# Optimization experiments

Measured on AMD Instinct MI355X. Metric: run time of the kernel, lower is better.

The kernel has to match this reference:

```python
import math
import jax, jax.numpy as jnp
import numpy as np

N_FREQS = 16
MAX_PERIOD = 4096.0
INJECTION_SCALE = 1.0


def setup_inputs() -> dict:
    key = jax.random.key(0)
    ks = jax.random.split(key, 5)
    B, L, D, K = 4, 8192, 1024, 2
    read_in = K * 2 * N_FREQS  # 64
    x = jax.random.normal(ks[0], (B, L, D), dtype=jnp.float32)
    # Linear weights stored as (in, out) so y = x @ W + b (== torch x @ W.T + b)
    inc_w = jax.random.normal(ks[1], (D, K), dtype=jnp.float32) * 0.02
    inc_b = jnp.full((K,), -2.0, dtype=jnp.float32)   # nn.init.constant_(inc_proj.bias, -2.0)
    reset_w = jax.random.normal(ks[2], (D, K), dtype=jnp.float32) * 0.02
    reset_b = jnp.full((K,), -5.0, dtype=jnp.float32)  # nn.init.constant_(reset_proj.bias, -5.0)
    read_w = jax.random.normal(ks[3], (read_in, D), dtype=jnp.float32) * 0.02
    read_b = jnp.zeros((D,), dtype=jnp.float32)
    return {"x": x, "inc_w": inc_w, "inc_b": inc_b, "reset_w": reset_w,
            "reset_b": reset_b, "read_w": read_w, "read_b": read_b}


def reference(x, inc_w, inc_b, reset_w, reset_b, read_w, read_b):
    # Gates from hidden state
    inc_logits = x @ inc_w + inc_b        # (B, L, K)
    reset_logits = x @ reset_w + reset_b  # (B, L, K)
    inc = jax.nn.sigmoid(inc_logits)
    keep = 1.0 - jax.nn.sigmoid(reset_logits)

    # Diagonal linear recurrence c[t] = keep[t]*c[t-1] + inc[t]
    # expressed as an associative scan over affine maps f(x) = k*x + i.
    def combine(left, right):
        kl, il = left
        kr, ir = right
        return (kl * kr, ir + kr * il)

    _, counters = jax.lax.associative_scan(combine, (keep, inc), axis=1)  # (B, L, K)

    # Sinusoidal readout: (B, L, K) -> (B, L, K*2*n_freqs)
    freqs = jnp.exp(jnp.linspace(0.0, math.log(MAX_PERIOD), N_FREQS)).astype(x.dtype)
    sc = counters[..., None] / freqs                       # (B, L, K, F)
    emb = jnp.concatenate([jnp.sin(sc), jnp.cos(sc)], -1)  # (B, L, K, 2F)
    B, L, K, _ = emb.shape
    emb = emb.reshape(B, L, K * 2 * N_FREQS)

    injection = INJECTION_SCALE * (emb @ read_w + read_b)  # (B, L, d_model)
    return injection, inc_logits, counters
```

## Files before the change

kernel.cpp:

```cpp
#include <hip/hip_runtime.h>

#define B_    4
#define L_    8192
#define D_    1024
#define ROWS_ 32768
#define NCH_  128

typedef __attribute__((ext_vector_type(8))) short  short8;
typedef __attribute__((ext_vector_type(4))) float  floatx4;

__device__ __forceinline__ unsigned short f2bf(float f){
  unsigned int u = __float_as_uint(f);
  u += 0x7fffu + ((u >> 16) & 1u);
  return (unsigned short)(u >> 16);
}

__global__ __launch_bounds__(512) void k_gates(
    const float* __restrict__ x,
    const float* __restrict__ inc_w, const float* __restrict__ inc_b,
    const float* __restrict__ reset_w, const float* __restrict__ reset_b,
    float* __restrict__ out_incl,
    float* __restrict__ cl, float* __restrict__ kc,
    float* __restrict__ sumP, float* __restrict__ sumQ,
    const float* __restrict__ read_w, unsigned short* __restrict__ Bt)
{
  const int blk  = blockIdx.x;
  if (blk >= 512){
    const int idx0 = ((blk - 512)*512 + threadIdx.x)*4;
    const int n  = idx0 >> 6;
    const int kk = idx0 & 63;
    ushort4 v;
    v.x = f2bf(read_w[(size_t)(kk+0)*D_ + n]);
    v.y = f2bf(read_w[(size_t)(kk+1)*D_ + n]);
    v.z = f2bf(read_w[(size_t)(kk+2)*D_ + n]);
    v.w = f2bf(read_w[(size_t)(kk+3)*D_ + n]);
    *(ushort4*)(Bt + idx0) = v;
    return;
  }

  __shared__ float s_keep[128];
  __shared__ float s_inc[128];
  const int b    = blk >> 7;
  const int ch   = blk & 127;
  const int tid  = threadIdx.x;
  const int w    = tid >> 6;
  const int lane = tid & 63;

  float4 wia[4], wib[4], wra[4], wrb[4];
  #pragma unroll
  for (int i = 0; i < 4; ++i){
    const int d0 = i*256 + lane*4;
    const float4* pi = (const float4*)(inc_w + d0*2);
    wia[i] = pi[0]; wib[i] = pi[1];
    const float4* pr = (const float4*)(reset_w + d0*2);
    wra[i] = pr[0]; wrb[i] = pr[1];
  }
  const float bi0 = inc_b[0], bi1 = inc_b[1];
  const float br0 = reset_b[0], br1 = reset_b[1];

  const int row0 = b*L_ + ch*64 + w*8;
  floatx4 xc[4], xn[4];
  {
    const floatx4* xr = (const floatx4*)(x + (size_t)row0 * D_);
    #pragma unroll
    for (int i = 0; i < 4; ++i) xc[i] = __builtin_nontemporal_load(xr + i*64 + lane);
  }
  #pragma unroll
  for (int r = 0; r < 8; ++r){
    if (r < 7){
      const floatx4* xr = (const floatx4*)(x + (size_t)(row0 + r + 1) * D_);
      #pragma unroll
      for (int i = 0; i < 4; ++i) xn[i] = __builtin_nontemporal_load(xr + i*64 + lane);
    }
    float ai0=0.f, ai1=0.f, ar0=0.f, ar1=0.f;
    #pragma unroll
    for (int i = 0; i < 4; ++i){
      const floatx4 v = xc[i];
      ai0 += v[0]*wia[i].x + v[1]*wia[i].z + v[2]*wib[i].x + v[3]*wib[i].z;
      ai1 += v[0]*wia[i].y + v[1]*wia[i].w + v[2]*wib[i].y + v[3]*wib[i].w;
      ar0 += v[0]*wra[i].x + v[1]*wra[i].z + v[2]*wrb[i].x + v[3]*wrb[i].z;
      ar1 += v[0]*wra[i].y + v[1]*wra[i].w + v[2]*wrb[i].y + v[3]*wrb[i].w;
    }
    #pragma unroll
    for (int m = 1; m < 64; m <<= 1){
      ai0 += __shfl_xor(ai0, m);
      ai1 += __shfl_xor(ai1, m);
      ar0 += __shfl_xor(ar0, m);
      ar1 += __shfl_xor(ar1, m);
    }
    if (lane == 0){
      const int row = row0 + r;
      const float il0 = ai0 + bi0, il1 = ai1 + bi1;
      const float rl0 = ar0 + br0, rl1 = ar1 + br1;
      out_incl[(size_t)row*2 + 0] = il0;
      out_incl[(size_t)row*2 + 1] = il1;
      const int lr = w*8 + r;
      s_inc [lr*2+0] = 1.f / (1.f + __expf(-il0));
      s_inc [lr*2+1] = 1.f / (1.f + __expf(-il1));
      s_keep[lr*2+0] = 1.f - 1.f / (1.f + __expf(-rl0));
      s_keep[lr*2+1] = 1.f - 1.f / (1.f + __expf(-rl1));
    }
    #pragma unroll
    for (int i = 0; i < 4; ++i) xc[i] = xn[i];
  }
  __syncthreads();

  if (tid < 128){
    const int k = w;
    float P = s_keep[lane*2 + k];
    float Q = s_inc [lane*2 + k];
    #pragma unroll
    for (int ofs = 1; ofs < 64; ofs <<= 1){
      const float Pp = __shfl_up(P, ofs);
      const float Qp = __shfl_up(Q, ofs);
      if (lane >= ofs){ Q = Q + P * Qp; P = P * Pp; }
    }
    const int row = b*L_ + ch*64 + lane;
    cl[(size_t)row*2 + k] = Q;
    kc[(size_t)row*2 + k] = P;
    if (lane == 63){
      const int seq = b*2 + k;
      sumP[seq*NCH_ + ch] = P;
      sumQ[seq*NCH_ + ch] = Q;
    }
  }
}

__global__ __launch_bounds__(256) void k_fused(
    const float* __restrict__ cl, const float* __restrict__ kc,
    const float* __restrict__ sumP, const float* __restrict__ sumQ,
    const unsigned short* __restrict__ Bt,
    const float* __restrict__ read_b,
    float* __restrict__ out_cnt, float* __restrict__ out)
{
  __shared__ float s_carry[2];
  const int tid  = threadIdx.x;
  const int w    = tid >> 6;
  const int lane = tid & 63;
  const int stripe = blockIdx.x >> 1;
  const int half   = blockIdx.x & 1;
  const int rowBase0 = stripe * 64;
  const int b  = rowBase0 >> 13;
  const int ch = stripe & 127;
  const int m    = lane & 15;
  const int quad = lane >> 4;
  const int colBase = half*512 + w*128;

  if (w < 2){
    const int seq = b*2 + w;
    const float* P0 = sumP + seq*NCH_;
    const float* Q0 = sumQ + seq*NCH_;
    float P = P0[lane], Q = Q0[lane];
    #pragma unroll
    for (int ofs = 1; ofs < 64; ofs <<= 1){
      const float Pp = __shfl_up(P, ofs);
      const float Qp = __shfl_up(Q, ofs);
      if (lane >= ofs){ Q = Q + P * Qp; P = P * Pp; }
    }
    float carry = 0.f;
    if (ch > 0 && ch <= 64) carry = __shfl(Q, ch-1);
    const float Qc = __shfl(Q, 63);
    float P2 = P0[64 + lane], Q2 = Q0[64 + lane];
    #pragma unroll
    for (int ofs = 1; ofs < 64; ofs <<= 1){
      const float Pp = __shfl_up(P2, ofs);
      const float Qp = __shfl_up(Q2, ofs);
      if (lane >= ofs){ Q2 = Q2 + P2 * Qp; P2 = P2 * Pp; }
    }
    Q2 = Q2 + P2 * Qc;
    if (ch >= 65) carry = __shfl(Q2, ch-65);
    if (lane == 0) s_carry[w] = carry;
  }
  __syncthreads();
  const float carry0 = s_carry[0];
  const float carry1 = s_carry[1];

  short8 b0[8], b1[8];
  float  bias[8];
  #pragma unroll
  for (int ct = 0; ct < 8; ++ct){
    const int n = colBase + ct*16 + m;
    const short8* bp = (const short8*)(Bt + (size_t)n * 64);
    b0[ct]  = bp[quad];
    b1[ct]  = bp[4 + quad];
    bias[ct] = read_b[n];
  }

  const float TWO_PI_INV = 0.15915494309189535f;
  const float STEP = 0.5743491774985175f;
  const float INVF0 = (quad & 1) ? 0.011841535573494211f  : 1.0f;
  const bool use_cos = (quad >> 1) != 0;

  #pragma unroll
  for (int rt = 0; rt < 4; ++rt){
    const int rowBase = rowBase0 + rt*16;
    const int row = rowBase + m;

    const float2 clv = *(const float2*)(cl + (size_t)row*2);
    const float2 kcv = *(const float2*)(kc + (size_t)row*2);
    const float c0 = clv.x + kcv.x * carry0;
    const float c1 = clv.y + kcv.y * carry1;
    if (half == 0 && w == 0 && lane < 16){
      ((float2*)out_cnt)[row] = make_float2(c0, c1);
    }

    float invf = INVF0;
    short8 a0, a1;
    #pragma unroll
    for (int j = 0; j < 8; ++j){
      float r0 = c0 * invf * TWO_PI_INV; r0 -= floorf(r0);
      float r1 = c1 * invf * TWO_PI_INV; r1 -= floorf(r1);
      const float e0 = use_cos ? __builtin_amdgcn_cosf(r0) : __builtin_amdgcn_sinf(r0);
      const float e1 = use_cos ? __builtin_amdgcn_cosf(r1) : __builtin_amdgcn_sinf(r1);
      a0[j] = (short)f2bf(e0);
      a1[j] = (short)f2bf(e1);
      invf *= STEP;
    }

    floatx4 acc[8];
    #pragma unroll
    for (int ct = 0; ct < 8; ++ct) acc[ct] = (floatx4){0.f,0.f,0.f,0.f};
    #pragma unroll
    for (int ct = 0; ct < 8; ++ct){
      acc[ct] = __builtin_amdgcn_mfma_f32_16x16x32_bf16(a0, b0[ct], acc[ct], 0, 0, 0);
      acc[ct] = __builtin_amdgcn_mfma_f32_16x16x32_bf16(a1, b1[ct], acc[ct], 0, 0, 0);
    }

    #pragma unroll
    for (int ct = 0; ct < 8; ++ct){
      const int col = colBase + ct*16 + m;
      #pragma unroll
      for (int r = 0; r < 4; ++r){
        const int orow = rowBase + quad*4 + r;
        __builtin_nontemporal_store(acc[ct][r] + bias[ct], &out[(size_t)orow*D_ + col]);
      }
    }
  }
}

extern "C" void kernel_launch(void* const* d_in, const int* in_sizes, int n_in,
                              void* d_out, int out_size, void* d_ws, size_t ws_size,
                              hipStream_t stream) {
  const float* x       = (const float*)d_in[0];
  const float* inc_w   = (const float*)d_in[1];
  const float* inc_b   = (const float*)d_in[2];
  const float* reset_w = (const float*)d_in[3];
  const float* reset_b = (const float*)d_in[4];
  const float* read_w  = (const float*)d_in[5];
  const float* read_b  = (const float*)d_in[6];

  float* out      = (float*)d_out;
  float* out_incl = out + (size_t)ROWS_ * D_;
  float* out_cnt  = out_incl + ROWS_ * 2;

  char* ws = (char*)d_ws;
  float* cl    = (float*)(ws + 0);
  float* kc    = (float*)(ws + 262144);
  float* sumP  = (float*)(ws + 524288);
  float* sumQ  = (float*)(ws + 528384);
  unsigned short* Bt  = (unsigned short*)(ws + 532480);

  k_gates<<<dim3(544),  dim3(512), 0, stream>>>(x, inc_w, inc_b, reset_w, reset_b,
                                                out_incl, cl, kc, sumP, sumQ,
                                                read_w, Bt);
  k_fused<<<dim3(1024), dim3(256), 0, stream>>>(cl, kc, sumP, sumQ, Bt, read_b,
                                                out_cnt, out);
}
```

Before: 253.3 us.

## Share sinusoidal A tiles via LDS and widen column tiles per wave in k_fused

Each block now covers all 1024 columns for a 64-row stripe, and each wave handles 256 columns instead of 128. The sin/cos embedding is computed once per row (one 16-row tile per wave) and shared through XOR-swizzled LDS, instead of being recomputed by every wave and by both half-blocks. The B-fragment and cl/kc loads are hoisted ahead of the carry scan so they overlap with it. In exchange it doubles the B registers per thread and halves the grid to 512 blocks, which may hurt occupancy despite the launch_bounds(256,2) hint.

```diff
diff --git a/kernel.cpp b/kernel.cpp
--- a/kernel.cpp
+++ b/kernel.cpp
@@ -126,7 +126,7 @@
   }
 }
 
-__global__ __launch_bounds__(256) void k_fused(
+__global__ __launch_bounds__(256, 2) void k_fused(
     const float* __restrict__ cl, const float* __restrict__ kc,
     const float* __restrict__ sumP, const float* __restrict__ sumQ,
     const unsigned short* __restrict__ Bt,
@@ -134,17 +134,31 @@
     float* __restrict__ out_cnt, float* __restrict__ out)
 {
   __shared__ float s_carry[2];
+  __shared__ unsigned short s_A[4][16][64];
   const int tid  = threadIdx.x;
   const int w    = tid >> 6;
   const int lane = tid & 63;
-  const int stripe = blockIdx.x >> 1;
-  const int half   = blockIdx.x & 1;
+  const int stripe = blockIdx.x;
   const int rowBase0 = stripe * 64;
   const int b  = rowBase0 >> 13;
   const int ch = stripe & 127;
   const int m    = lane & 15;
   const int quad = lane >> 4;
-  const int colBase = half*512 + w*128;
+  const int colBase = w * 256;
+
+  short8 b0[16], b1[16];
+  float  bias[16];
+  #pragma unroll
+  for (int ct = 0; ct < 16; ++ct){
+    const int n = colBase + ct*16 + m;
+    const short8* bp = (const short8*)(Bt + (size_t)n * 64);
+    b0[ct]  = bp[quad];
+    b1[ct]  = bp[4 + quad];
+    bias[ct] = read_b[n];
+  }
+  const int arow = rowBase0 + w*16 + m;
+  const float2 clv = *(const float2*)(cl + (size_t)arow*2);
+  const float2 kcv = *(const float2*)(kc + (size_t)arow*2);
 
   if (w < 2){
     const int seq = b*2 + w;
@@ -175,59 +189,51 @@
   const float carry0 = s_carry[0];
   const float carry1 = s_carry[1];
 
-  short8 b0[8], b1[8];
-  float  bias[8];
-  #pragma unroll
-  for (int ct = 0; ct < 8; ++ct){
-    const int n = colBase + ct*16 + m;
-    const short8* bp = (const short8*)(Bt + (size_t)n * 64);
-    b0[ct]  = bp[quad];
-    b1[ct]  = bp[4 + quad];
-    bias[ct] = read_b[n];
-  }
-
-  const float TWO_PI_INV = 0.15915494309189535f;
-  const float STEP = 0.5743491774985175f;
-  const float INVF0 = (quad & 1) ? 0.011841535573494211f  : 1.0f;
-  const bool use_cos = (quad >> 1) != 0;
-
-  #pragma unroll
-  for (int rt = 0; rt < 4; ++rt){
-    const int rowBase = rowBase0 + rt*16;
-    const int row = rowBase + m;
-
-    const float2 clv = *(const float2*)(cl + (size_t)row*2);
-    const float2 kcv = *(const float2*)(kc + (size_t)row*2);
+  {
     const float c0 = clv.x + kcv.x * carry0;
     const float c1 = clv.y + kcv.y * carry1;
-    if (half == 0 && w == 0 && lane < 16){
-      ((float2*)out_cnt)[row] = make_float2(c0, c1);
-    }
-
-    float invf = INVF0;
-    short8 a0, a1;
+    if (quad == 0){
+      ((float2*)out_cnt)[arow] = make_float2(c0, c1);
+    }
+    const float TWO_PI_INV = 0.15915494309189535f;
+    const float STEP = 0.5743491774985175f;
+    float invf = (quad & 1) ? 0.011841535573494211f  : 1.0f;
+    const bool use_cos = (quad >> 1) != 0;
+    short8 a0v, a1v;
     #pragma unroll
     for (int j = 0; j < 8; ++j){
       float r0 = c0 * invf * TWO_PI_INV; r0 -= floorf(r0);
       float r1 = c1 * invf * TWO_PI_INV; r1 -= floorf(r1);
       const float e0 = use_cos ? __builtin_amdgcn_cosf(r0) : __builtin_amdgcn_sinf(r0);
       const float e1 = use_cos ? __builtin_amdgcn_cosf(r1) : __builtin_amdgcn_sinf(r1);
-      a0[j] = (short)f2bf(e0);
-      a1[j] = (short)f2bf(e1);
+      a0v[j] = (short)f2bf(e0);
+      a1v[j] = (short)f2bf(e1);
       invf *= STEP;
     }
-
-    floatx4 acc[8];
-    #pragma unroll
-    for (int ct = 0; ct < 8; ++ct) acc[ct] = (floatx4){0.f,0.f,0.f,0.f};
-    #pragma unroll
-    for (int ct = 0; ct < 8; ++ct){
+    const int h = m & 7;
+    *(short8*)&s_A[w][m][((quad    ) ^ h) * 8] = a0v;
+    *(short8*)&s_A[w][m][((4 + quad) ^ h) * 8] = a1v;
+  }
+  __syncthreads();
+
+  const int h = m & 7;
+  #pragma unroll
+  for (int rt = 0; rt < 4; ++rt){
+    const short8 a0 = *(const short8*)&s_A[rt][m][((quad    ) ^ h) * 8];
+    const short8 a1 = *(const short8*)&s_A[rt][m][((4 + quad) ^ h) * 8];
+
+    floatx4 acc[16];
+    #pragma unroll
+    for (int ct = 0; ct < 16; ++ct) acc[ct] = (floatx4){0.f,0.f,0.f,0.f};
+    #pragma unroll
+    for (int ct = 0; ct < 16; ++ct){
       acc[ct] = __builtin_amdgcn_mfma_f32_16x16x32_bf16(a0, b0[ct], acc[ct], 0, 0, 0);
       acc[ct] = __builtin_amdgcn_mfma_f32_16x16x32_bf16(a1, b1[ct], acc[ct], 0, 0, 0);
     }
 
-    #pragma unroll
-    for (int ct = 0; ct < 8; ++ct){
+    const int rowBase = rowBase0 + rt*16;
+    #pragma unroll
+    for (int ct = 0; ct < 16; ++ct){
       const int col = colBase + ct*16 + m;
       #pragma unroll
       for (int r = 0; r < 4; ++r){
@@ -263,6 +269,6 @@
   k_gates<<<dim3(544),  dim3(512), 0, stream>>>(x, inc_w, inc_b, reset_w, reset_b,
                                                 out_incl, cl, kc, sumP, sumQ,
                                                 read_w, Bt);
-  k_fused<<<dim3(1024), dim3(256), 0, stream>>>(cl, kc, sumP, sumQ, Bt, read_b,
+  k_fused<<<dim3(512),  dim3(256), 0, stream>>>(cl, kc, sumP, sumQ, Bt, read_b,
                                                 out_cnt, out);
 }
```

Result: slower. 271.7 us (+7.2%).
